# Optimization experiments

Hardware: AMD Instinct MI355X
Metric: run time of the kernel (lower is better)

Reference implementation:

```python
import jax, jax.numpy as jnp
import numpy as np

EPS = 1e-3  # keras LayerNormalization default epsilon

def layer_norm(x, gamma, beta):
    mu = jnp.mean(x, axis=-1, keepdims=True)
    var = jnp.var(x, axis=-1, keepdims=True)
    return (x - mu) * jax.lax.rsqrt(var + EPS) * gamma + beta

def setup_inputs() -> dict:
    key = jax.random.key(0)
    ks = jax.random.split(key, 10)
    B, N, FD, AD, PD, DP = 4, 512, 256, 256, 128, 64
    s = lambda k, *sh: jax.random.normal(k, sh, dtype=jnp.float32)
    return {
        "F": s(ks[0], B, N, FD),
        "D": s(ks[1], B, N, N, DP),
        "Wq": s(ks[2], FD, AD) / np.sqrt(FD),
        "Wk": s(ks[3], FD, AD) / np.sqrt(FD),
        "Wv": s(ks[4], FD, AD) / np.sqrt(FD),
        "g_f": jnp.ones((FD,), jnp.float32),
        "b_f": jnp.zeros((FD,), jnp.float32),
        "g_p": jnp.ones((DP,), jnp.float32),
        "b_p": jnp.zeros((DP,), jnp.float32),
        "W_pt": s(ks[5], DP, PD) / np.sqrt(DP),
        "b_pt": jnp.zeros((PD,), jnp.float32),
        "W_ph": s(ks[6], PD, 1) / np.sqrt(PD),
    }

def reference(F, D, Wq, Wk, Wv, g_f, b_f, g_p, b_p, W_pt, b_pt, W_ph):
    # features path
    Fn = layer_norm(F, g_f, b_f)                       # [B,N,FD]
    Q = Fn @ Wq                                        # [B,N,AD]
    K = Fn @ Wk
    V = Fn @ Wv
    # pair-bias path: LN -> Dense(pairs_dim)+bias -> Dense(num_heads=1)
    Bn = layer_norm(D, g_p, b_p)                       # [B,N,N,DP]
    Bt = Bn @ W_pt + b_pt                              # [B,N,N,PD]
    bias = (Bt @ W_ph)[..., 0]                         # [B,N,N]
    scalar = 1.0 / jnp.sqrt(jnp.float32(Q.shape[-1]))
    A = jnp.einsum('bqd,bkd->bqk', Q, K) + bias        # QK^T + pair bias
    A = jax.nn.softmax(scalar * A, axis=-1)
    O = jnp.einsum('bqk,bkd->bqd', A, V)               # [B,N,AD]
    return jnp.sum(O, axis=-1)                         # [B,N]
```

## Files before the change

kernel.cpp:

```cpp
#include <hip/hip_runtime.h>
#include <cstddef>
#include <cstdint>

#define OFF_GW    0
#define OFF_WV    64
#define OFF_SC    320
#define OFF_VSUM  384
#define OFF_Q     2432
#define OFF_K     526720

typedef float v4f __attribute__((ext_vector_type(4)));

__device__ __forceinline__ void load_lds_16B(const float* g, float* l) {
  __builtin_amdgcn_global_load_lds(
      (const __attribute__((address_space(1))) uint32_t*)g,
      (__attribute__((address_space(3))) uint32_t*)l, 16, 0, 0);
}

__global__ __launch_bounds__(256) void k0_consts(
    const float* __restrict__ Wv, const float* __restrict__ g_p,
    const float* __restrict__ b_p, const float* __restrict__ W_pt,
    const float* __restrict__ b_pt, const float* __restrict__ W_ph,
    float* __restrict__ ws) {
  int t = threadIdx.x;
  if (blockIdx.x < 64) {
    int row = blockIdx.x * 4 + (t >> 6);
    int l = t & 63;
    float s = 0.f;
#pragma unroll
    for (int j = 0; j < 4; ++j) s += Wv[row * 256 + l + 64 * j];
    for (int m = 32; m >= 1; m >>= 1) s += __shfl_xor(s, m);
    if (l == 0) ws[OFF_WV + row] = s;
  } else {
    __shared__ float wc_s[64];
    __shared__ float wph_s[128];
    if (t < 128) wph_s[t] = W_ph[t];
    __syncthreads();
    int c = t >> 2, sub = t & 3;
    float wc = 0.f;
#pragma unroll
    for (int j = 0; j < 32; ++j)
      wc += W_pt[c * 128 + sub * 32 + j] * wph_s[sub * 32 + j];
    wc += __shfl_xor(wc, 1);
    wc += __shfl_xor(wc, 2);
    if (sub == 0) {
      wc_s[c] = wc;
      ws[OFF_GW + c] = g_p[c] * wc;
    }
    __syncthreads();
    if (t == 0) {
      float sg = 0.f, bc = 0.f;
      for (int cc = 0; cc < 64; ++cc) {
        sg += g_p[cc] * wc_s[cc];
        bc += b_p[cc] * wc_s[cc];
      }
      for (int p = 0; p < 128; ++p) bc += b_pt[p] * wph_s[p];
      ws[OFF_SC] = sg;
      ws[OFF_SC + 1] = bc;
    }
  }
}

__global__ __launch_bounds__(256) void k1_ln_qk(
    const float* __restrict__ F, const float* __restrict__ Wq,
    const float* __restrict__ Wk, const float* __restrict__ g_f,
    const float* __restrict__ b_f, float* __restrict__ ws) {
  __shared__ __align__(16) float fn[8][260];
  __shared__ float smu[8], srn[8];
  int t = threadIdx.x;
  int g = blockIdx.x >> 1, h = blockIdx.x & 1;
  int row0 = g * 8;
  const float* Fp = F + (size_t)row0 * 256;
#pragma unroll
  for (int k = 0; k < 8; ++k) fn[k][t] = Fp[k * 256 + t];
  __syncthreads();
  int r = t >> 5, l32 = t & 31;
  float s1 = 0.f, s2 = 0.f;
#pragma unroll
  for (int m = 0; m < 8; ++m) {
    float x = fn[r][l32 + 32 * m];
    s1 += x;
    s2 += x * x;
  }
  for (int m = 16; m >= 1; m >>= 1) {
    s1 += __shfl_xor(s1, m);
    s2 += __shfl_xor(s2, m);
  }
  if (l32 == 0) {
    float mu = s1 * (1.f / 256.f);
    float var = s2 * (1.f / 256.f) - mu * mu;
    smu[r] = mu;
    srn[r] = rsqrtf(var + 1e-3f);
  }
  __syncthreads();
  float gf = g_f[t], bf = b_f[t];
#pragma unroll
  for (int k = 0; k < 8; ++k)
    fn[k][t] = (fn[k][t] - smu[k]) * srn[k] * gf + bf;
  __syncthreads();
  if (h == 0) {
    const float* wv = ws + OFF_WV;
    float s = 0.f;
#pragma unroll
    for (int m = 0; m < 8; ++m) s += fn[r][l32 + 32 * m] * wv[l32 + 32 * m];
    for (int m = 16; m >= 1; m >>= 1) s += __shfl_xor(s, m);
    if (l32 == 0) ws[OFF_VSUM + row0 + r] = s;
  }
  int matsel = t >> 7;
  int col = h * 128 + (t & 127);
  const float* W = matsel ? Wk : Wq;
  float acc[8] = {0, 0, 0, 0, 0, 0, 0, 0};
#pragma unroll 2
  for (int f = 0; f < 256; f += 4) {
    float w0 = W[(f + 0) * 256 + col];
    float w1 = W[(f + 1) * 256 + col];
    float w2 = W[(f + 2) * 256 + col];
    float w3 = W[(f + 3) * 256 + col];
#pragma unroll
    for (int k = 0; k < 8; ++k) {
      v4f x = *(const v4f*)(&fn[k][f]);
      acc[k] = fmaf(x.w, w3,
               fmaf(x.z, w2, fmaf(x.y, w1, fmaf(x.x, w0, acc[k]))));
    }
  }
  float* Out = ws + (matsel ? OFF_K : OFF_Q) + (size_t)row0 * 256 + col;
#pragma unroll
  for (int k = 0; k < 8; ++k) Out[k * 256] = acc[k];
}

__global__ __launch_bounds__(256) void kb_bias_attn(
    const float* __restrict__ D, const float* __restrict__ ws,
    float* __restrict__ out) {
  __shared__ __align__(16) float stage[4][2][1024];
  __shared__ float Sx[4][512];
  __shared__ __align__(16) float Qs[4][256];
  __shared__ float vs[512];
  int t = threadIdx.x;
  int w = t >> 6, l = t & 63;
  int b = blockIdx.x >> 7, tile = blockIdx.x & 127;
  int rowbase = b * 512 + tile * 4;

#pragma unroll
  for (int k = 0; k < 4; ++k)
    Qs[k][t] = ws[OFF_Q + (size_t)(rowbase + k) * 256 + t];
  vs[t] = ws[OFF_VSUM + b * 512 + t];
  vs[t + 256] = ws[OFF_VSUM + b * 512 + 256 + t];
  float sum_gw = ws[OFF_SC];
  float bconst = ws[OFF_SC + 1];
  int qq = l & 3, e4 = l >> 2;
  v4f g_rot[4];
#pragma unroll
  for (int j = 0; j < 4; ++j) {
    int p = (e4 + j) & 3;
    g_rot[j] = *(const v4f*)(ws + OFF_GW + qq * 16 + p * 4);
  }
  __syncthreads();

  const float* Dw = D + (size_t)(rowbase + w) * 512 * 64;
  float* buf0 = &stage[w][0][0];
  float* buf1 = &stage[w][1][0];
#pragma unroll
  for (int j = 0; j < 4; ++j)
    load_lds_16B(Dw + j * 256 + l * 4, buf0 + j * 256);

  for (int i = 0; i < 32; ++i) {
    float* cur = (i & 1) ? buf1 : buf0;
    float* nxt = (i & 1) ? buf0 : buf1;
    if (i + 1 < 32) {
#pragma unroll
      for (int j = 0; j < 4; ++j)
        load_lds_16B(Dw + (i + 1) * 1024 + j * 256 + l * 4, nxt + j * 256);
      __builtin_amdgcn_s_waitcnt(0x0F74);
    } else {
      __builtin_amdgcn_s_waitcnt(0x0F70);
    }
    asm volatile("" ::: "memory");
    const float* ebase = cur + e4 * 64 + qq * 16;
    float s1 = 0.f, s2 = 0.f, sw = 0.f;
#pragma unroll
    for (int j = 0; j < 4; ++j) {
      int p = (e4 + j) & 3;
      v4f x = *(const v4f*)(ebase + p * 4);
      s1 += x.x + x.y + x.z + x.w;
      s2 += x.x * x.x + x.y * x.y + x.z * x.z + x.w * x.w;
      sw += x.x * g_rot[j].x + x.y * g_rot[j].y + x.z * g_rot[j].z +
            x.w * g_rot[j].w;
    }
    s1 += __shfl_xor(s1, 1);
    s2 += __shfl_xor(s2, 1);
    sw += __shfl_xor(sw, 1);
    s1 += __shfl_xor(s1, 2);
    s2 += __shfl_xor(s2, 2);
    sw += __shfl_xor(sw, 2);
    if (qq == 0) {
      float mu = s1 * (1.f / 64.f);
      float var = s2 * (1.f / 64.f) - mu * mu;
      float rn = rsqrtf(var + 1e-3f);
      Sx[w][i * 16 + e4] = (rn * (sw - mu * sum_gw) + bconst) * 0.0625f;
    }
  }
  __syncthreads();

  const float* Kg = ws + OFF_K;
  const v4f* K0p = (const v4f*)(Kg + (size_t)(b * 512 + t) * 256);
  const v4f* K1p = (const v4f*)(Kg + (size_t)(b * 512 + 256 + t) * 256);
  float a0[4] = {0, 0, 0, 0}, a1[4] = {0, 0, 0, 0};
#pragma unroll 8
  for (int f = 0; f < 64; ++f) {
    v4f kv0 = K0p[f];
    v4f kv1 = K1p[f];
#pragma unroll
    for (int rr = 0; rr < 4; ++rr) {
      v4f qv = *(const v4f*)(&Qs[rr][f * 4]);
      a0[rr] += qv.x * kv0.x + qv.y * kv0.y + qv.z * kv0.z + qv.w * kv0.w;
      a1[rr] += qv.x * kv1.x + qv.y * kv1.y + qv.z * kv1.z + qv.w * kv1.w;
    }
  }
#pragma unroll
  for (int rr = 0; rr < 4; ++rr) {
    Sx[rr][t] += a0[rr] * 0.0625f;
    Sx[rr][t + 256] += a1[rr] * 0.0625f;
  }
  __syncthreads();

  float m = -1e30f;
#pragma unroll
  for (int j = 0; j < 8; ++j) m = fmaxf(m, Sx[w][l + 64 * j]);
  for (int mm = 32; mm >= 1; mm >>= 1) m = fmaxf(m, __shfl_xor(m, mm));
  float se = 0.f, sv = 0.f;
#pragma unroll
  for (int j = 0; j < 8; ++j) {
    float ev = __expf(Sx[w][l + 64 * j] - m);
    se += ev;
    sv += ev * vs[l + 64 * j];
  }
  for (int mm = 32; mm >= 1; mm >>= 1) {
    se += __shfl_xor(se, mm);
    sv += __shfl_xor(sv, mm);
  }
  if (l == 0) out[rowbase + w] = sv / se;
}

extern "C" void kernel_launch(void* const* d_in, const int* in_sizes, int n_in,
                              void* d_out, int out_size, void* d_ws,
                              size_t ws_size, hipStream_t stream) {
  const float* F    = (const float*)d_in[0];
  const float* D    = (const float*)d_in[1];
  const float* Wq   = (const float*)d_in[2];
  const float* Wk   = (const float*)d_in[3];
  const float* Wv   = (const float*)d_in[4];
  const float* g_f  = (const float*)d_in[5];
  const float* b_f  = (const float*)d_in[6];
  const float* g_p  = (const float*)d_in[7];
  const float* b_p  = (const float*)d_in[8];
  const float* W_pt = (const float*)d_in[9];
  const float* b_pt = (const float*)d_in[10];
  const float* W_ph = (const float*)d_in[11];
  float* out = (float*)d_out;
  float* ws = (float*)d_ws;

  k0_consts<<<65, 256, 0, stream>>>(Wv, g_p, b_p, W_pt, b_pt, W_ph, ws);
  k1_ln_qk<<<512, 256, 0, stream>>>(F, Wq, Wk, g_f, b_f, ws);
  kb_bias_attn<<<512, 256, 0, stream>>>(D, ws, out);
}
```

Measured before the change: 439.0 us.

## Deepen D prefetch to 4-stage ring and vectorize Q/K projection per block

The pair-bias kernel's per-wave LDS staging grows from a double buffer to a 4-slot ring that keeps three chunks of D in flight, with the vmcnt waits adjusted to match. The goal is to hide more HBM latency on the dominant D stream. The Q/K projection kernel now has each block compute all 256 columns for 8 rows, using float4 weight loads and 4-row vector accumulators, so it launches half as many blocks and LN runs once per row group instead of twice. The trade-offs are more LDS per block for staging, which can lower occupancy, and fewer blocks for the projection.

```diff
diff --git a/kernel.cpp b/kernel.cpp
--- a/kernel.cpp
+++ b/kernel.cpp
@@ -68,37 +68,40 @@
   __shared__ __align__(16) float fn[8][260];
   __shared__ float smu[8], srn[8];
   int t = threadIdx.x;
-  int g = blockIdx.x >> 1, h = blockIdx.x & 1;
-  int row0 = g * 8;
+  int row0 = blockIdx.x * 8;
   const float* Fp = F + (size_t)row0 * 256;
 #pragma unroll
   for (int k = 0; k < 8; ++k) fn[k][t] = Fp[k * 256 + t];
   __syncthreads();
   int r = t >> 5, l32 = t & 31;
-  float s1 = 0.f, s2 = 0.f;
-#pragma unroll
-  for (int m = 0; m < 8; ++m) {
-    float x = fn[r][l32 + 32 * m];
-    s1 += x;
-    s2 += x * x;
-  }
-  for (int m = 16; m >= 1; m >>= 1) {
-    s1 += __shfl_xor(s1, m);
-    s2 += __shfl_xor(s2, m);
-  }
-  if (l32 == 0) {
-    float mu = s1 * (1.f / 256.f);
-    float var = s2 * (1.f / 256.f) - mu * mu;
-    smu[r] = mu;
-    srn[r] = rsqrtf(var + 1e-3f);
-  }
-  __syncthreads();
-  float gf = g_f[t], bf = b_f[t];
-#pragma unroll
-  for (int k = 0; k < 8; ++k)
-    fn[k][t] = (fn[k][t] - smu[k]) * srn[k] * gf + bf;
-  __syncthreads();
-  if (h == 0) {
+  {
+    float s1 = 0.f, s2 = 0.f;
+#pragma unroll
+    for (int m = 0; m < 8; ++m) {
+      float x = fn[r][l32 + 32 * m];
+      s1 += x;
+      s2 += x * x;
+    }
+    for (int m = 16; m >= 1; m >>= 1) {
+      s1 += __shfl_xor(s1, m);
+      s2 += __shfl_xor(s2, m);
+    }
+    if (l32 == 0) {
+      float mu = s1 * (1.f / 256.f);
+      float var = s2 * (1.f / 256.f) - mu * mu;
+      smu[r] = mu;
+      srn[r] = rsqrtf(var + 1e-3f);
+    }
+  }
+  __syncthreads();
+  {
+    float gf = g_f[t], bf = b_f[t];
+#pragma unroll
+    for (int k = 0; k < 8; ++k)
+      fn[k][t] = (fn[k][t] - smu[k]) * srn[k] * gf + bf;
+  }
+  __syncthreads();
+  {
     const float* wv = ws + OFF_WV;
     float s = 0.f;
 #pragma unroll
@@ -106,32 +109,39 @@
     for (int m = 16; m >= 1; m >>= 1) s += __shfl_xor(s, m);
     if (l32 == 0) ws[OFF_VSUM + row0 + r] = s;
   }
-  int matsel = t >> 7;
-  int col = h * 128 + (t & 127);
-  const float* W = matsel ? Wk : Wq;
-  float acc[8] = {0, 0, 0, 0, 0, 0, 0, 0};
+  int w = t >> 6, l = t & 63;
+  int mat = w >> 1;
+  int rbase = (w & 1) * 4;
+  const float* wp = (mat ? Wk : Wq) + 4 * l;
+  v4f acc0 = {0, 0, 0, 0}, acc1 = {0, 0, 0, 0};
+  v4f acc2 = {0, 0, 0, 0}, acc3 = {0, 0, 0, 0};
 #pragma unroll 2
   for (int f = 0; f < 256; f += 4) {
-    float w0 = W[(f + 0) * 256 + col];
-    float w1 = W[(f + 1) * 256 + col];
-    float w2 = W[(f + 2) * 256 + col];
-    float w3 = W[(f + 3) * 256 + col];
-#pragma unroll
-    for (int k = 0; k < 8; ++k) {
-      v4f x = *(const v4f*)(&fn[k][f]);
-      acc[k] = fmaf(x.w, w3,
-               fmaf(x.z, w2, fmaf(x.y, w1, fmaf(x.x, w0, acc[k]))));
-    }
-  }
-  float* Out = ws + (matsel ? OFF_K : OFF_Q) + (size_t)row0 * 256 + col;
-#pragma unroll
-  for (int k = 0; k < 8; ++k) Out[k * 256] = acc[k];
+    v4f x0 = *(const v4f*)(&fn[rbase + 0][f]);
+    v4f x1 = *(const v4f*)(&fn[rbase + 1][f]);
+    v4f x2 = *(const v4f*)(&fn[rbase + 2][f]);
+    v4f x3 = *(const v4f*)(&fn[rbase + 3][f]);
+    v4f w0 = *(const v4f*)(wp + (size_t)(f + 0) * 256);
+    v4f w1 = *(const v4f*)(wp + (size_t)(f + 1) * 256);
+    v4f w2 = *(const v4f*)(wp + (size_t)(f + 2) * 256);
+    v4f w3 = *(const v4f*)(wp + (size_t)(f + 3) * 256);
+    acc0 += w0 * x0.x + w1 * x0.y + w2 * x0.z + w3 * x0.w;
+    acc1 += w0 * x1.x + w1 * x1.y + w2 * x1.z + w3 * x1.w;
+    acc2 += w0 * x2.x + w1 * x2.y + w2 * x2.z + w3 * x2.w;
+    acc3 += w0 * x3.x + w1 * x3.y + w2 * x3.z + w3 * x3.w;
+  }
+  float* Out =
+      ws + (mat ? OFF_K : OFF_Q) + (size_t)(row0 + rbase) * 256 + 4 * l;
+  *(v4f*)(Out + 0 * 256) = acc0;
+  *(v4f*)(Out + 1 * 256) = acc1;
+  *(v4f*)(Out + 2 * 256) = acc2;
+  *(v4f*)(Out + 3 * 256) = acc3;
 }
 
 __global__ __launch_bounds__(256) void kb_bias_attn(
     const float* __restrict__ D, const float* __restrict__ ws,
     float* __restrict__ out) {
-  __shared__ __align__(16) float stage[4][2][1024];
+  __shared__ __align__(16) float stage[4][4][1024];
   __shared__ float Sx[4][512];
   __shared__ __align__(16) float Qs[4][256];
   __shared__ float vs[512];
@@ -157,25 +167,29 @@
   __syncthreads();
 
   const float* Dw = D + (size_t)(rowbase + w) * 512 * 64;
-  float* buf0 = &stage[w][0][0];
-  float* buf1 = &stage[w][1][0];
-#pragma unroll
-  for (int j = 0; j < 4; ++j)
-    load_lds_16B(Dw + j * 256 + l * 4, buf0 + j * 256);
+#pragma unroll
+  for (int c = 0; c < 3; ++c)
+#pragma unroll
+    for (int j = 0; j < 4; ++j)
+      load_lds_16B(Dw + c * 1024 + j * 256 + l * 4, &stage[w][c][j * 256]);
 
   for (int i = 0; i < 32; ++i) {
-    float* cur = (i & 1) ? buf1 : buf0;
-    float* nxt = (i & 1) ? buf0 : buf1;
-    if (i + 1 < 32) {
+    if (i + 3 < 32) {
+      float* nxt = &stage[w][(i + 3) & 3][0];
 #pragma unroll
       for (int j = 0; j < 4; ++j)
-        load_lds_16B(Dw + (i + 1) * 1024 + j * 256 + l * 4, nxt + j * 256);
+        load_lds_16B(Dw + (size_t)(i + 3) * 1024 + j * 256 + l * 4,
+                     nxt + j * 256);
+      __builtin_amdgcn_s_waitcnt(0x0F7C);
+    } else if (i == 29) {
+      __builtin_amdgcn_s_waitcnt(0x0F78);
+    } else if (i == 30) {
       __builtin_amdgcn_s_waitcnt(0x0F74);
     } else {
       __builtin_amdgcn_s_waitcnt(0x0F70);
     }
     asm volatile("" ::: "memory");
-    const float* ebase = cur + e4 * 64 + qq * 16;
+    const float* ebase = &stage[w][i & 3][0] + e4 * 64 + qq * 16;
     float s1 = 0.f, s2 = 0.f, sw = 0.f;
 #pragma unroll
     for (int j = 0; j < 4; ++j) {
@@ -260,6 +274,6 @@
   float* ws = (float*)d_ws;
 
   k0_consts<<<65, 256, 0, stream>>>(Wv, g_p, b_p, W_pt, b_pt, W_ph, ws);
-  k1_ln_qk<<<512, 256, 0, stream>>>(F, Wq, Wk, g_f, b_f, ws);
+  k1_ln_qk<<<256, 256, 0, stream>>>(F, Wq, Wk, g_f, b_f, ws);
   kb_bias_attn<<<512, 256, 0, stream>>>(D, ws, out);
 }
```

After: 482.8 us. 10.0% more time.
